# Performance work log

Measured on AMD Instinct MI355X. Metric: run time of the kernel, lower is better.

The kernel has to match this reference:

```python
import jax, jax.numpy as jnp
import numpy as np

H = 8      # num_attention_heads
DH = 96    # attention_head_size
LN_EPS = 1e-5


def setup_inputs() -> dict:
    key = jax.random.key(0)
    ks = jax.random.split(key, 12)
    B, S, D = 2, 768, 768
    sc = 0.02
    return {
        "hidden_states": jax.random.normal(ks[0], (B, S, D), jnp.float32),
        "distance_matrix": jax.random.uniform(ks[1], (B, S, S), jnp.float32) * 20.0,
        "angle_matrix": jax.random.uniform(ks[2], (B, S, S), jnp.float32) * np.pi,
        "attention_mask": jnp.ones((B, S), jnp.float32),
        "Wq": jax.random.normal(ks[3], (D, D), jnp.float32) * sc,
        "bq": jnp.zeros((D,), jnp.float32),
        "Wk": jax.random.normal(ks[4], (D, D), jnp.float32) * sc,
        "bk": jnp.zeros((D,), jnp.float32),
        "Wv": jax.random.normal(ks[5], (D, D), jnp.float32) * sc,
        "bv": jnp.zeros((D,), jnp.float32),
        "Wd": jax.random.normal(ks[6], (DH,), jnp.float32) * sc,
        "bd": jnp.zeros((DH,), jnp.float32),
        "Wa": jax.random.normal(ks[7], (DH,), jnp.float32) * sc,
        "ba": jnp.zeros((DH,), jnp.float32),
        "Wo": jax.random.normal(ks[8], (D, D), jnp.float32) * sc,
        "bo": jnp.zeros((D,), jnp.float32),
        "ln_g": jnp.ones((D,), jnp.float32),
        "ln_b": jnp.zeros((D,), jnp.float32),
    }


def _heads(x, B, S):
    # [B,S,D] -> [B,H,S,DH]
    return x.reshape(B, S, H, DH).transpose(0, 2, 1, 3)


def reference(hidden_states, distance_matrix, angle_matrix, attention_mask,
              Wq, bq, Wk, bk, Wv, bv, Wd, bd, Wa, ba, Wo, bo, ln_g, ln_b):
    B, S, D = hidden_states.shape
    q = _heads(hidden_states @ Wq.T + bq, B, S)   # [B,H,S,DH]
    k = _heads(hidden_states @ Wk.T + bk, B, S)
    v = _heads(hidden_states @ Wv.T + bv, B, S)

    scores = jnp.einsum('bhid,bhjd->bhij', q, k) / jnp.sqrt(jnp.float32(DH))

    # distance / angle relative-position biases: emb[b,i,j,:] = dist[b,i,j]*Wd + bd
    dist_emb = distance_matrix[..., None] * Wd + bd   # [B,S,S,DH]
    scores = scores + jnp.einsum('bhid,bijd->bhij', q, dist_emb)
    ang_emb = angle_matrix[..., None] * Wa + ba       # [B,S,S,DH]
    scores = scores + jnp.einsum('bhid,bijd->bhij', q, ang_emb)

    # key mask, broadcast over heads and query positions
    scores = scores + (1.0 - attention_mask)[:, None, None, :] * -10000.0

    probs = jax.nn.softmax(scores, axis=-1)           # [B,H,S,S]
    ctx = jnp.einsum('bhij,bhjd->bhid', probs, v)
    ctx = ctx.transpose(0, 2, 1, 3).reshape(B, S, D)  # [B,S,D]

    out = ctx @ Wo.T + bo
    x = out + hidden_states
    mu = jnp.mean(x, axis=-1, keepdims=True)
    var = jnp.var(x, axis=-1, keepdims=True)
    out = (x - mu) * jax.lax.rsqrt(var + LN_EPS) * ln_g + ln_b
    return out, probs
```

## Files before the change

### kernel.cpp

```cpp
#include <hip/hip_runtime.h>
#include <stdint.h>

#define B_  2
#define S_  768
#define D_  768
#define H_  8
#define DH_ 96

typedef unsigned short ushort_t;
typedef __bf16 bf16x8 __attribute__((ext_vector_type(8)));
typedef float  f32x4  __attribute__((ext_vector_type(4)));

__device__ inline ushort_t f2bf(float f) {
    union { float f; unsigned int u; } v; v.f = f;
    unsigned int u = v.u;
    unsigned int r = u + 0x7fffu + ((u >> 16) & 1u);
    return (ushort_t)(r >> 16);
}
__device__ inline float bf2f(ushort_t u) {
    union { unsigned int i; float f; } c; c.i = ((unsigned int)u) << 16;
    return c.f;
}

__device__ inline void glds16(const void* gp, void* lp) {
    auto g = reinterpret_cast<const __attribute__((address_space(1))) uint32_t*>(
        reinterpret_cast<uintptr_t>(gp));
    auto l = reinterpret_cast<__attribute__((address_space(3))) uint32_t*>(
        reinterpret_cast<uintptr_t>(lp));
    __builtin_amdgcn_global_load_lds(g, l, 16, 0, 0);
}

__global__ __launch_bounds__(256) void k_convert(
        const float* __restrict__ X, const float* __restrict__ Wq,
        const float* __restrict__ Wk, const float* __restrict__ Wv,
        const float* __restrict__ Wo,
        ushort_t* __restrict__ Xb, ushort_t* __restrict__ Wb) {
    const int NX4 = (B_ * S_ * D_) / 4;
    const int NW4 = (D_ * D_) / 4;
    int i = blockIdx.x * blockDim.x + threadIdx.x;
    float4 v;
    ushort_t* dst;
    if (i < NX4) {
        v = ((const float4*)X)[i];
        dst = Xb + i * 4;
    } else {
        int wi = i - NX4;
        int sel = wi / NW4;
        int off = wi - sel * NW4;
        const float* src = (sel == 0) ? Wq : (sel == 1) ? Wk : (sel == 2) ? Wv : Wo;
        v = ((const float4*)src)[off];
        dst = Wb + wi * 4;
    }
    ushort4 o;
    o.x = f2bf(v.x); o.y = f2bf(v.y); o.z = f2bf(v.z); o.w = f2bf(v.w);
    *(ushort4*)dst = o;
}

__device__ inline void gemm64_dbuf(
        const ushort_t* __restrict__ A, int lda,
        const ushort_t* __restrict__ Bt, int ldb,
        int K, int m0, int n0,
        ushort_t* As, ushort_t* Bs, f32x4 acc[2][2]) {
    const int tid  = threadIdx.x;
    const int lane = tid & 63, wave = tid >> 6;
    const int wm = (wave >> 1) * 32, wn = (wave & 1) * 32;
    const int fr = lane & 15, fk = (lane >> 4) * 8;
    const ushort_t* Ap = A  + (size_t)(m0 + wave * 16 + (lane >> 2)) * lda + (lane & 3) * 8;
    const ushort_t* Bp = Bt + (size_t)(n0 + wave * 16 + (lane >> 2)) * ldb + (lane & 3) * 8;
    glds16(Ap, As + wave * 512);
    glds16(Bp, Bs + wave * 512);
    for (int kt = 0; kt < K; kt += 32) {
        const int cur = (kt >> 5) & 1;
        __syncthreads();
        if (kt + 32 < K) {
            glds16(Ap + kt + 32, As + (cur ^ 1) * 2048 + wave * 512);
            glds16(Bp + kt + 32, Bs + (cur ^ 1) * 2048 + wave * 512);
        }
        const ushort_t* Ab = As + cur * 2048;
        const ushort_t* Bb = Bs + cur * 2048;
        bf16x8 a0 = *(const bf16x8*)&Ab[(wm      + fr) * 32 + fk];
        bf16x8 a1 = *(const bf16x8*)&Ab[(wm + 16 + fr) * 32 + fk];
        bf16x8 b0 = *(const bf16x8*)&Bb[(wn      + fr) * 32 + fk];
        bf16x8 b1 = *(const bf16x8*)&Bb[(wn + 16 + fr) * 32 + fk];
        acc[0][0] = __builtin_amdgcn_mfma_f32_16x16x32_bf16(a0, b0, acc[0][0], 0, 0, 0);
        acc[0][1] = __builtin_amdgcn_mfma_f32_16x16x32_bf16(a0, b1, acc[0][1], 0, 0, 0);
        acc[1][0] = __builtin_amdgcn_mfma_f32_16x16x32_bf16(a1, b0, acc[1][0], 0, 0, 0);
        acc[1][1] = __builtin_amdgcn_mfma_f32_16x16x32_bf16(a1, b1, acc[1][1], 0, 0, 0);
    }
}

__global__ __launch_bounds__(256) void k_qkv(
        const ushort_t* __restrict__ Xb, const ushort_t* __restrict__ Wb,
        const float* __restrict__ bq, const float* __restrict__ bk,
        const float* __restrict__ bv,
        ushort_t* __restrict__ Qb, ushort_t* __restrict__ Kb,
        ushort_t* __restrict__ Vtb) {
    __shared__ __align__(16) ushort_t As[2 * 64 * 32];
    __shared__ __align__(16) ushort_t Bs[2 * 64 * 32];
    f32x4 acc[2][2];
    #pragma unroll
    for (int i = 0; i < 2; i++)
        #pragma unroll
        for (int j = 0; j < 2; j++) acc[i][j] = (f32x4){0.f, 0.f, 0.f, 0.f};
    const int m0 = blockIdx.y * 64, n0 = blockIdx.x * 64;
    gemm64_dbuf(Xb, D_, Wb, D_, D_, m0, n0, As, Bs, acc);
    const int lane = threadIdx.x & 63, wave = threadIdx.x >> 6;
    const int wm = (wave >> 1) * 32, wn = (wave & 1) * 32;
    #pragma unroll
    for (int ni = 0; ni < 2; ni++) {
        int gcol = n0 + wn + ni * 16 + (lane & 15);
        int gsel = gcol / D_, d768 = gcol - gsel * D_;
        int h = d768 / DH_, d = d768 - h * DH_;
        float bias = (gsel == 0 ? bq : (gsel == 1 ? bk : bv))[d768];
        #pragma unroll
        for (int mi = 0; mi < 2; mi++) {
            int grow0 = m0 + wm + mi * 16 + (lane >> 4) * 4;
            int b = grow0 / S_, s0 = grow0 - b * S_;
            int bh = b * H_ + h;
            if (gsel == 2) {
                ushort4 o4;
                o4.x = f2bf(acc[mi][ni][0] + bias);
                o4.y = f2bf(acc[mi][ni][1] + bias);
                o4.z = f2bf(acc[mi][ni][2] + bias);
                o4.w = f2bf(acc[mi][ni][3] + bias);
                *(ushort4*)&Vtb[((size_t)bh * DH_ + d) * S_ + s0] = o4;
            } else if (gsel == 1) {
                #pragma unroll
                for (int r = 0; r < 4; r++) {
                    ushort_t ob = f2bf(acc[mi][ni][r] + bias);
                    Kb[(((size_t)bh * 12 + (d >> 3)) * S_ + s0 + r) * 8 + (d & 7)] = ob;
                }
            } else {
                #pragma unroll
                for (int r = 0; r < 4; r++) {
                    ushort_t ob = f2bf(acc[mi][ni][r] + bias);
                    Qb[((size_t)bh * S_ + s0 + r) * DH_ + d] = ob;
                }
            }
        }
    }
}

__global__ __launch_bounds__(256) void k_qcoef(
        const ushort_t* __restrict__ Qb,
        const float* __restrict__ Wd, const float* __restrict__ bd,
        const float* __restrict__ Wa, const float* __restrict__ ba,
        float* __restrict__ qcoef) {
    const int wave = threadIdx.x >> 6, lane = threadIdx.x & 63;
    const int row = blockIdx.x * 4 + wave;
    const ushort_t* q = Qb + (size_t)row * DH_;
    float e0 = bf2f(q[lane]);
    float c0 = e0 * Wd[lane];
    float c1 = e0 * Wa[lane];
    float c2 = e0 * (bd[lane] + ba[lane]);
    if (lane < 32) {
        int d = 64 + lane;
        float e1 = bf2f(q[d]);
        c0 += e1 * Wd[d];
        c1 += e1 * Wa[d];
        c2 += e1 * (bd[d] + ba[d]);
    }
    #pragma unroll
    for (int o = 32; o > 0; o >>= 1) {
        c0 += __shfl_down(c0, o);
        c1 += __shfl_down(c1, o);
        c2 += __shfl_down(c2, o);
    }
    if (lane == 0) {
        qcoef[row * 3 + 0] = c0;
        qcoef[row * 3 + 1] = c1;
        qcoef[row * 3 + 2] = c2;
    }
}

#define FL1B 20480
#define VBUF 24576
__global__ __launch_bounds__(256, 3) void k_flash(
        const ushort_t* __restrict__ Qb, const ushort_t* __restrict__ Kb,
        const ushort_t* __restrict__ Vtb, const float* __restrict__ qcoef,
        const float* __restrict__ distm, const float* __restrict__ angm,
        const float* __restrict__ mask,
        float* __restrict__ probs, ushort_t* __restrict__ Ctxb) {
    __shared__ __align__(16) char sm[2 * VBUF + 512];
    float* mstat = (float*)(sm + 2 * VBUF);
    float* lstat = (float*)(sm + 2 * VBUF + 256);
    const int idx = blockIdx.x;
    const int h = idx / 96, rem = idx - h * 96;
    const int b = rem / 48, r0 = (rem - b * 48) * 16;
    const int bh = b * H_ + h;
    const int tid = threadIdx.x, lane = tid & 63, w = tid >> 6;
    const int frn = lane & 15, g = lane >> 4;
    const ushort_t* Qbh = Qb + (size_t)bh * S_ * DH_;
    const ushort_t* Kbh = Kb + (size_t)bh * 12 * S_ * 8;
    const ushort_t* Vbh = Vtb + (size_t)bh * DH_ * S_;

    auto stage = [&](int c) {
        char* bufc = sm + (c & 1) * FL1B;
        ushort_t* Ks = (ushort_t*)bufc;
        #pragma unroll
        for (int t = 0; t < 3; ++t) {
            int grp = w * 3 + t;
            glds16(Kbh + (((size_t)grp * S_ + c * 64 + lane) << 3), Ks + grp * 512);
        }
        int row = 4 * w + g;
        int colb = (frn ^ (row & 7)) << 2;
        size_t src = ((size_t)b * S_ + r0 + row) * S_ + c * 64 + colb;
        glds16(distm + src, (float*)(bufc + 12288) + w * 256);
        glds16(angm  + src, (float*)(bufc + 16384) + w * 256);
    };
    auto stage_v = [&](int p) {
        ushort_t* Vs = (ushort_t*)(sm + (p & 1) * VBUF);
        const int c0 = p * 128;
        #pragma unroll
        for (int t = 0; t < 6; ++t) {
            int q = w * 6 + t;
            int d = 4 * q + (lane >> 4);
            int ug = (lane & 15) ^ (d & 15);
            glds16(Vbh + (size_t)d * S_ + c0 + ug * 8, Vs + q * 512);
        }
    };

    stage(0);

    bf16x8 aq0, aq1, aq2;
    {
        const ushort_t* qp = Qbh + (size_t)(r0 + frn) * DH_ + g * 8;
        aq0 = *(const bf16x8*)qp;
        aq1 = *(const bf16x8*)(qp + 32);
        aq2 = *(const bf16x8*)(qp + 64);
    }
    float qc0, qc1, qc2;
    {
        const float* qp = qcoef + ((size_t)bh * S_ + r0 + frn) * 3;
        qc0 = qp[0]; qc1 = qp[1]; qc2 = qp[2];
    }
    const float isq = 0.10206207261596577f;
    const int dswz = ((4 * w + g) ^ (frn & 7)) << 2;
    const int jrow = (16 * w + frn) * 8;

    f32x4 acc[12];
    __syncthreads();
    #pragma unroll
    for (int c = 0; c < 12; ++c) {
        if (c < 11) stage(c + 1);
        char* bufc = sm + (c & 1) * FL1B;
        const ushort_t* Ks = (const ushort_t*)bufc;
        const float* Dd = (const float*)(bufc + 12288);
        const float* Da = (const float*)(bufc + 16384);
        bf16x8 k0 = *(const bf16x8*)&Ks[(g    ) * 512 + jrow];
        bf16x8 k1 = *(const bf16x8*)&Ks[(g + 4) * 512 + jrow];
        bf16x8 k2 = *(const bf16x8*)&Ks[(g + 8) * 512 + jrow];
        f32x4 ca = (f32x4){0.f, 0.f, 0.f, 0.f};
        ca = __builtin_amdgcn_mfma_f32_16x16x32_bf16(k0, aq0, ca, 0, 0, 0);
        ca = __builtin_amdgcn_mfma_f32_16x16x32_bf16(k1, aq1, ca, 0, 0, 0);
        ca = __builtin_amdgcn_mfma_f32_16x16x32_bf16(k2, aq2, ca, 0, 0, 0);
        float4 d4 = *(const float4*)(Dd + frn * 64 + dswz);
        float4 a4 = *(const float4*)(Da + frn * 64 + dswz);
        float4 m4 = *(const float4*)(mask + b * S_ + c * 64 + w * 16 + g * 4);
        f32x4 o;
        o[0] = ca[0] * isq + d4.x * qc0 + a4.x * qc1 + qc2 + (1.f - m4.x) * -10000.f;
        o[1] = ca[1] * isq + d4.y * qc0 + a4.y * qc1 + qc2 + (1.f - m4.y) * -10000.f;
        o[2] = ca[2] * isq + d4.z * qc0 + a4.z * qc1 + qc2 + (1.f - m4.z) * -10000.f;
        o[3] = ca[3] * isq + d4.w * qc0 + a4.w * qc1 + qc2 + (1.f - m4.w) * -10000.f;
        acc[c] = o;
        __syncthreads();
    }

    stage_v(0);
    float mx = -1e30f;
    #pragma unroll
    for (int c = 0; c < 12; ++c)
        #pragma unroll
        for (int r = 0; r < 4; ++r) mx = fmaxf(mx, acc[c][r]);
    mx = fmaxf(mx, __shfl_xor(mx, 16));
    mx = fmaxf(mx, __shfl_xor(mx, 32));
    if (g == 0) mstat[w * 16 + frn] = mx;
    __syncthreads();
    float mf = fmaxf(fmaxf(mstat[frn], mstat[16 + frn]),
                     fmaxf(mstat[32 + frn], mstat[48 + frn]));
    float sum = 0.f;
    #pragma unroll
    for (int c = 0; c < 12; ++c)
        #pragma unroll
        for (int r = 0; r < 4; ++r) {
            float e = __expf(acc[c][r] - mf);
            acc[c][r] = e;
            sum += e;
        }
    sum += __shfl_xor(sum, 16);
    sum += __shfl_xor(sum, 32);
    if (g == 0) lstat[w * 16 + frn] = sum;
    __syncthreads();
    float inv = 1.f / (lstat[frn] + lstat[16 + frn] + lstat[32 + frn] + lstat[48 + frn]);

    f32x4 accO[6];
    #pragma unroll
    for (int i = 0; i < 6; ++i) accO[i] = (f32x4){0.f, 0.f, 0.f, 0.f};
    float* prow = probs + ((size_t)bh * S_ + r0 + frn) * S_ + w * 16 + g * 4;
    const int vsub = (g & 1) << 2;
    const int u0 = 2 * w + (g >> 1);
    #pragma unroll
    for (int p = 0; p < 6; ++p) {
        if (p < 5) stage_v(p + 1);
        const ushort_t* Vs = (const ushort_t*)(sm + (p & 1) * VBUF);
        const int c = 2 * p;
        float4 pw;
        pw.x = acc[c][0] * inv; pw.y = acc[c][1] * inv;
        pw.z = acc[c][2] * inv; pw.w = acc[c][3] * inv;
        *(float4*)(prow + c * 64) = pw;
        pw.x = acc[c + 1][0] * inv; pw.y = acc[c + 1][1] * inv;
        pw.z = acc[c + 1][2] * inv; pw.w = acc[c + 1][3] * inv;
        *(float4*)(prow + (c + 1) * 64) = pw;
        union { bf16x8 v; ushort_t u[8]; } pa;
        #pragma unroll
        for (int r = 0; r < 4; ++r) {
            pa.u[r]     = f2bf(acc[c][r]);
            pa.u[r + 4] = f2bf(acc[c + 1][r]);
        }
        #pragma unroll
        for (int nt = 0; nt < 6; ++nt) {
            int d = nt * 16 + frn;
            const ushort_t* vr = Vs + d * 128 + vsub;
            union { bf16x8 v; uint2 q2[2]; } vb;
            vb.q2[0] = *(const uint2*)(vr + (((u0    ) ^ frn) << 3));
            vb.q2[1] = *(const uint2*)(vr + (((u0 + 8) ^ frn) << 3));
            accO[nt] = __builtin_amdgcn_mfma_f32_16x16x32_bf16(pa.v, vb.v, accO[nt], 0, 0, 0);
        }
        __syncthreads();
    }

    float* ctxred = (float*)sm;
    {
        int zr = tid >> 4, zc = tid & 15;
        #pragma unroll
        for (int i = 0; i < 6; ++i) ctxred[zr * 100 + i * 16 + zc] = 0.f;
    }
    __syncthreads();
    #pragma unroll
    for (int nt = 0; nt < 6; ++nt)
        #pragma unroll
        for (int r = 0; r < 4; ++r)
            atomicAdd(&ctxred[(4 * g + r) * 100 + nt * 16 + frn], accO[nt][r]);
    __syncthreads();
    {
        int zr = tid >> 4, zc = tid & 15;
        float ivr = 1.f / (lstat[zr] + lstat[16 + zr] + lstat[32 + zr] + lstat[48 + zr]);
        ushort_t* crow = Ctxb + ((size_t)b * S_ + r0 + zr) * D_ + h * DH_;
        #pragma unroll
        for (int i = 0; i < 6; ++i)
            crow[i * 16 + zc] = f2bf(ctxred[zr * 100 + i * 16 + zc] * ivr);
    }
}

__global__ __launch_bounds__(256) void k_out(
        const ushort_t* __restrict__ Ctxb, const ushort_t* __restrict__ Wob,
        const float* __restrict__ bo, const float* __restrict__ hidden,
        float* __restrict__ xbuf) {
    __shared__ __align__(16) ushort_t As[2 * 64 * 32];
    __shared__ __align__(16) ushort_t Bs[2 * 64 * 32];
    f32x4 acc[2][2];
    #pragma unroll
    for (int i = 0; i < 2; i++)
        #pragma unroll
        for (int j = 0; j < 2; j++) acc[i][j] = (f32x4){0.f, 0.f, 0.f, 0.f};
    const int m0 = blockIdx.y * 64, n0 = blockIdx.x * 64;
    gemm64_dbuf(Ctxb, D_, Wob, D_, D_, m0, n0, As, Bs, acc);
    const int lane = threadIdx.x & 63, wave = threadIdx.x >> 6;
    const int wm = (wave >> 1) * 32, wn = (wave & 1) * 32;
    #pragma unroll
    for (int ni = 0; ni < 2; ni++) {
        int gcol = n0 + wn + ni * 16 + (lane & 15);
        float bias = bo[gcol];
        #pragma unroll
        for (int mi = 0; mi < 2; mi++) {
            #pragma unroll
            for (int r = 0; r < 4; r++) {
                int grow = m0 + wm + mi * 16 + (lane >> 4) * 4 + r;
                xbuf[(size_t)grow * D_ + gcol] =
                    acc[mi][ni][r] + bias + hidden[(size_t)grow * D_ + gcol];
            }
        }
    }
}

__global__ __launch_bounds__(256) void k_ln(
        const float* __restrict__ xbuf, const float* __restrict__ g,
        const float* __restrict__ bb, float* __restrict__ out) {
    const float* x = xbuf + (size_t)blockIdx.x * D_;
    const int t = threadIdx.x;
    float a0 = x[t], a1 = x[t + 256], a2 = x[t + 512];
    float s = a0 + a1 + a2;
    float ss = a0 * a0 + a1 * a1 + a2 * a2;
    __shared__ float r1[4], r2[4];
    #pragma unroll
    for (int o = 32; o > 0; o >>= 1) { s += __shfl_down(s, o); ss += __shfl_down(ss, o); }
    if ((t & 63) == 0) { r1[t >> 6] = s; r2[t >> 6] = ss; }
    __syncthreads();
    float ts = r1[0] + r1[1] + r1[2] + r1[3];
    float tss = r2[0] + r2[1] + r2[2] + r2[3];
    float mu = ts * (1.0f / D_);
    float var = tss * (1.0f / D_) - mu * mu;
    float rstd = rsqrtf(var + 1e-5f);
    float* o = out + (size_t)blockIdx.x * D_;
    o[t]       = (a0 - mu) * rstd * g[t]       + bb[t];
    o[t + 256] = (a1 - mu) * rstd * g[t + 256] + bb[t + 256];
    o[t + 512] = (a2 - mu) * rstd * g[t + 512] + bb[t + 512];
}

extern "C" void kernel_launch(void* const* d_in, const int* in_sizes, int n_in,
                              void* d_out, int out_size, void* d_ws, size_t ws_size,
                              hipStream_t stream) {
    const float* X     = (const float*)d_in[0];
    const float* distm = (const float*)d_in[1];
    const float* angm  = (const float*)d_in[2];
    const float* mask  = (const float*)d_in[3];
    const float* Wq    = (const float*)d_in[4];
    const float* bq    = (const float*)d_in[5];
    const float* Wk    = (const float*)d_in[6];
    const float* bk    = (const float*)d_in[7];
    const float* Wv    = (const float*)d_in[8];
    const float* bv    = (const float*)d_in[9];
    const float* Wd    = (const float*)d_in[10];
    const float* bd    = (const float*)d_in[11];
    const float* Wa    = (const float*)d_in[12];
    const float* ba    = (const float*)d_in[13];
    const float* Wo    = (const float*)d_in[14];
    const float* bo    = (const float*)d_in[15];
    const float* ln_g  = (const float*)d_in[16];
    const float* ln_b  = (const float*)d_in[17];

    float* outp  = (float*)d_out;
    float* probs = (float*)d_out + (size_t)B_ * S_ * D_;

    char* ws = (char*)d_ws;
    ushort_t* Xb    = (ushort_t*)(ws + 0);
    ushort_t* Wb    = (ushort_t*)(ws + 2359296);
    ushort_t* Qb    = (ushort_t*)(ws + 7077888);
    ushort_t* Kb    = (ushort_t*)(ws + 9437184);
    ushort_t* Vtb   = (ushort_t*)(ws + 11796480);
    ushort_t* Ctxb  = (ushort_t*)(ws + 14155776);
    float*    qcoef = (float*)   (ws + 16515072);
    float*    xbuf  = (float*)   (ws + 16662528);

    k_convert<<<3456, 256, 0, stream>>>(X, Wq, Wk, Wv, Wo, Xb, Wb);
    k_qkv<<<dim3(36, 24), 256, 0, stream>>>(Xb, Wb, bq, bk, bv, Qb, Kb, Vtb);
    k_qcoef<<<3072, 256, 0, stream>>>(Qb, Wd, bd, Wa, ba, qcoef);
    k_flash<<<768, 256, 0, stream>>>(Qb, Kb, Vtb, qcoef, distm, angm, mask, probs, Ctxb);
    k_out<<<dim3(12, 24), 256, 0, stream>>>(Ctxb, Wb + (size_t)2304 * 768, bo, X, xbuf);
    k_ln<<<1536, 256, 0, stream>>>(xbuf, ln_g, ln_b, outp);
}
```

Baseline: 190.6 us.

## Pre-convert distance/angle matrices to fp16, enlarge QKV GEMM tiles, remap flash blocks

The distance and angle matrices are converted to fp16 in the conversion kernel, so the attention kernel stages half as many bytes per tile through LDS, using a new swizzle. The QKV projection moves from 64x64 to 128x128 tiles with a 4x4 MFMA fragment grid per wave for more data reuse. The flash kernel's block index now interleaves batch and head in its low bits. The extra conversion pass reads the fp32 matrices and writes fp16 copies, which adds global traffic that may cancel the savings, and fp16 rounding slightly perturbs the bias terms.

```diff
diff --git a/kernel.cpp b/kernel.cpp
--- a/kernel.cpp
+++ b/kernel.cpp
@@ -10,6 +10,7 @@
 typedef unsigned short ushort_t;
 typedef __bf16 bf16x8 __attribute__((ext_vector_type(8)));
 typedef float  f32x4  __attribute__((ext_vector_type(4)));
+typedef _Float16 f16x4 __attribute__((ext_vector_type(4)));
 
 __device__ inline ushort_t f2bf(float f) {
     union { float f; unsigned int u; } v; v.f = f;
@@ -20,6 +21,9 @@
 __device__ inline float bf2f(ushort_t u) {
     union { unsigned int i; float f; } c; c.i = ((unsigned int)u) << 16;
     return c.f;
+}
+__device__ inline ushort_t f2h(float f) {
+    union { _Float16 h; ushort_t u; } c; c.h = (_Float16)f; return c.u;
 }
 
 __device__ inline void glds16(const void* gp, void* lp) {
@@ -33,26 +37,40 @@
 __global__ __launch_bounds__(256) void k_convert(
         const float* __restrict__ X, const float* __restrict__ Wq,
         const float* __restrict__ Wk, const float* __restrict__ Wv,
-        const float* __restrict__ Wo,
-        ushort_t* __restrict__ Xb, ushort_t* __restrict__ Wb) {
+        const float* __restrict__ Wo, const float* __restrict__ distm,
+        const float* __restrict__ angm,
+        ushort_t* __restrict__ Xb, ushort_t* __restrict__ Wb,
+        ushort_t* __restrict__ Dh, ushort_t* __restrict__ Ah) {
     const int NX4 = (B_ * S_ * D_) / 4;
     const int NW4 = (D_ * D_) / 4;
+    const int NWall = 4 * NW4;
+    const int ND4 = (B_ * S_ * S_) / 4;
     int i = blockIdx.x * blockDim.x + threadIdx.x;
     float4 v;
     ushort_t* dst;
+    bool h16 = false;
     if (i < NX4) {
         v = ((const float4*)X)[i];
         dst = Xb + i * 4;
-    } else {
+    } else if (i < NX4 + NWall) {
         int wi = i - NX4;
         int sel = wi / NW4;
         int off = wi - sel * NW4;
         const float* src = (sel == 0) ? Wq : (sel == 1) ? Wk : (sel == 2) ? Wv : Wo;
         v = ((const float4*)src)[off];
         dst = Wb + wi * 4;
+    } else if (i < NX4 + NWall + ND4) {
+        int off = i - NX4 - NWall;
+        v = ((const float4*)distm)[off];
+        dst = Dh + off * 4; h16 = true;
+    } else {
+        int off = i - NX4 - NWall - ND4;
+        v = ((const float4*)angm)[off];
+        dst = Ah + off * 4; h16 = true;
     }
     ushort4 o;
-    o.x = f2bf(v.x); o.y = f2bf(v.y); o.z = f2bf(v.z); o.w = f2bf(v.w);
+    if (h16) { o.x = f2h(v.x); o.y = f2h(v.y); o.z = f2h(v.z); o.w = f2h(v.w); }
+    else     { o.x = f2bf(v.x); o.y = f2bf(v.y); o.z = f2bf(v.z); o.w = f2bf(v.w); }
     *(ushort4*)dst = o;
 }
 
@@ -95,47 +113,71 @@
         const float* __restrict__ bv,
         ushort_t* __restrict__ Qb, ushort_t* __restrict__ Kb,
         ushort_t* __restrict__ Vtb) {
-    __shared__ __align__(16) ushort_t As[2 * 64 * 32];
-    __shared__ __align__(16) ushort_t Bs[2 * 64 * 32];
-    f32x4 acc[2][2];
-    #pragma unroll
-    for (int i = 0; i < 2; i++)
-        #pragma unroll
-        for (int j = 0; j < 2; j++) acc[i][j] = (f32x4){0.f, 0.f, 0.f, 0.f};
-    const int m0 = blockIdx.y * 64, n0 = blockIdx.x * 64;
-    gemm64_dbuf(Xb, D_, Wb, D_, D_, m0, n0, As, Bs, acc);
-    const int lane = threadIdx.x & 63, wave = threadIdx.x >> 6;
-    const int wm = (wave >> 1) * 32, wn = (wave & 1) * 32;
-    #pragma unroll
-    for (int ni = 0; ni < 2; ni++) {
-        int gcol = n0 + wn + ni * 16 + (lane & 15);
+    __shared__ __align__(16) ushort_t As[2][128 * 32];
+    __shared__ __align__(16) ushort_t Bs[2][128 * 32];
+    const int tid = threadIdx.x, lane = tid & 63, w = tid >> 6;
+    const int m0 = blockIdx.y * 128, n0 = blockIdx.x * 128;
+    const int frn = lane & 15, fko = (lane >> 4) * 8, frg4 = (lane >> 4) * 4;
+    const int wm = (w >> 1) * 64, wn = (w & 1) * 64;
+    const int srow = lane >> 2, scol = (lane & 3) * 8;
+    f32x4 acc[4][4];
+    #pragma unroll
+    for (int i = 0; i < 4; i++)
+        #pragma unroll
+        for (int j = 0; j < 4; j++) acc[i][j] = (f32x4){0.f, 0.f, 0.f, 0.f};
+    auto stageAB = [&](int kt, int buf) {
+        #pragma unroll
+        for (int t = 0; t < 2; ++t) {
+            int ins = w * 2 + t;
+            int row = ins * 16 + srow;
+            glds16(Xb + (size_t)(m0 + row) * D_ + kt + scol, &As[buf][ins * 512]);
+            glds16(Wb + (size_t)(n0 + row) * D_ + kt + scol, &Bs[buf][ins * 512]);
+        }
+    };
+    stageAB(0, 0);
+    for (int kt = 0; kt < D_; kt += 32) {
+        const int cur = (kt >> 5) & 1;
+        __syncthreads();
+        if (kt + 32 < D_) stageAB(kt + 32, cur ^ 1);
+        bf16x8 af[4], bfr[4];
+        #pragma unroll
+        for (int i = 0; i < 4; ++i) {
+            af[i]  = *(const bf16x8*)&As[cur][(wm + i * 16 + frn) * 32 + fko];
+            bfr[i] = *(const bf16x8*)&Bs[cur][(wn + i * 16 + frn) * 32 + fko];
+        }
+        #pragma unroll
+        for (int i = 0; i < 4; ++i)
+            #pragma unroll
+            for (int j = 0; j < 4; ++j)
+                acc[i][j] = __builtin_amdgcn_mfma_f32_16x16x32_bf16(af[i], bfr[j], acc[i][j], 0, 0, 0);
+    }
+    #pragma unroll
+    for (int j = 0; j < 4; ++j) {
+        int gcol = n0 + wn + j * 16 + frn;
         int gsel = gcol / D_, d768 = gcol - gsel * D_;
         int h = d768 / DH_, d = d768 - h * DH_;
         float bias = (gsel == 0 ? bq : (gsel == 1 ? bk : bv))[d768];
         #pragma unroll
-        for (int mi = 0; mi < 2; mi++) {
-            int grow0 = m0 + wm + mi * 16 + (lane >> 4) * 4;
+        for (int i = 0; i < 4; ++i) {
+            int grow0 = m0 + wm + i * 16 + frg4;
             int b = grow0 / S_, s0 = grow0 - b * S_;
             int bh = b * H_ + h;
             if (gsel == 2) {
                 ushort4 o4;
-                o4.x = f2bf(acc[mi][ni][0] + bias);
-                o4.y = f2bf(acc[mi][ni][1] + bias);
-                o4.z = f2bf(acc[mi][ni][2] + bias);
-                o4.w = f2bf(acc[mi][ni][3] + bias);
+                o4.x = f2bf(acc[i][j][0] + bias);
+                o4.y = f2bf(acc[i][j][1] + bias);
+                o4.z = f2bf(acc[i][j][2] + bias);
+                o4.w = f2bf(acc[i][j][3] + bias);
                 *(ushort4*)&Vtb[((size_t)bh * DH_ + d) * S_ + s0] = o4;
             } else if (gsel == 1) {
                 #pragma unroll
-                for (int r = 0; r < 4; r++) {
-                    ushort_t ob = f2bf(acc[mi][ni][r] + bias);
-                    Kb[(((size_t)bh * 12 + (d >> 3)) * S_ + s0 + r) * 8 + (d & 7)] = ob;
-                }
+                for (int r = 0; r < 4; r++)
+                    Kb[(((size_t)bh * 12 + (d >> 3)) * S_ + s0 + r) * 8 + (d & 7)] =
+                        f2bf(acc[i][j][r] + bias);
             } else {
                 #pragma unroll
-                for (int r = 0; r < 4; r++) {
-                    ushort_t ob = f2bf(acc[mi][ni][r] + bias);
-                    Qb[((size_t)bh * S_ + s0 + r) * DH_ + d] = ob;
-                }
+                for (int r = 0; r < 4; r++)
+                    Qb[((size_t)bh * S_ + s0 + r) * DH_ + d] = f2bf(acc[i][j][r] + bias);
             }
         }
     }
@@ -173,21 +215,21 @@
     }
 }
 
-#define FL1B 20480
+#define FL1B 16384
 #define VBUF 24576
 __global__ __launch_bounds__(256, 3) void k_flash(
         const ushort_t* __restrict__ Qb, const ushort_t* __restrict__ Kb,
         const ushort_t* __restrict__ Vtb, const float* __restrict__ qcoef,
-        const float* __restrict__ distm, const float* __restrict__ angm,
+        const ushort_t* __restrict__ Dh, const ushort_t* __restrict__ Ah,
         const float* __restrict__ mask,
         float* __restrict__ probs, ushort_t* __restrict__ Ctxb) {
     __shared__ __align__(16) char sm[2 * VBUF + 512];
     float* mstat = (float*)(sm + 2 * VBUF);
     float* lstat = (float*)(sm + 2 * VBUF + 256);
     const int idx = blockIdx.x;
-    const int h = idx / 96, rem = idx - h * 96;
-    const int b = rem / 48, r0 = (rem - b * 48) * 16;
-    const int bh = b * H_ + h;
+    const int bh = idx & 15, t = idx >> 4;
+    const int b = bh >> 3, h = bh & 7;
+    const int r0 = t * 16;
     const int tid = threadIdx.x, lane = tid & 63, w = tid >> 6;
     const int frn = lane & 15, g = lane >> 4;
     const ushort_t* Qbh = Qb + (size_t)bh * S_ * DH_;
@@ -198,22 +240,22 @@
         char* bufc = sm + (c & 1) * FL1B;
         ushort_t* Ks = (ushort_t*)bufc;
         #pragma unroll
-        for (int t = 0; t < 3; ++t) {
-            int grp = w * 3 + t;
+        for (int tt = 0; tt < 3; ++tt) {
+            int grp = w * 3 + tt;
             glds16(Kbh + (((size_t)grp * S_ + c * 64 + lane) << 3), Ks + grp * 512);
         }
-        int row = 4 * w + g;
-        int colb = (frn ^ (row & 7)) << 2;
-        size_t src = ((size_t)b * S_ + r0 + row) * S_ + c * 64 + colb;
-        glds16(distm + src, (float*)(bufc + 12288) + w * 256);
-        glds16(angm  + src, (float*)(bufc + 16384) + w * 256);
+        int row8 = ((w & 1) << 3) + (lane >> 3);
+        int usrc = (2 * (lane & 7)) ^ (row8 & 14);
+        const ushort_t* srcm = (w >> 1) ? Ah : Dh;
+        glds16(srcm + ((size_t)(b * S_ + r0 + row8)) * S_ + c * 64 + usrc * 4,
+               bufc + 12288 + ((w >> 1) << 11) + ((w & 1) << 10));
     };
     auto stage_v = [&](int p) {
         ushort_t* Vs = (ushort_t*)(sm + (p & 1) * VBUF);
         const int c0 = p * 128;
         #pragma unroll
-        for (int t = 0; t < 6; ++t) {
-            int q = w * 6 + t;
+        for (int tt = 0; tt < 6; ++tt) {
+            int q = w * 6 + tt;
             int d = 4 * q + (lane >> 4);
             int ug = (lane & 15) ^ (d & 15);
             glds16(Vbh + (size_t)d * S_ + c0 + ug * 8, Vs + q * 512);
@@ -235,7 +277,7 @@
         qc0 = qp[0]; qc1 = qp[1]; qc2 = qp[2];
     }
     const float isq = 0.10206207261596577f;
-    const int dswz = ((4 * w + g) ^ (frn & 7)) << 2;
+    const int daswz = (((w * 4 + g) ^ (frn & 14)) << 2);
     const int jrow = (16 * w + frn) * 8;
 
     f32x4 acc[12];
@@ -245,8 +287,6 @@
         if (c < 11) stage(c + 1);
         char* bufc = sm + (c & 1) * FL1B;
         const ushort_t* Ks = (const ushort_t*)bufc;
-        const float* Dd = (const float*)(bufc + 12288);
-        const float* Da = (const float*)(bufc + 16384);
         bf16x8 k0 = *(const bf16x8*)&Ks[(g    ) * 512 + jrow];
         bf16x8 k1 = *(const bf16x8*)&Ks[(g + 4) * 512 + jrow];
         bf16x8 k2 = *(const bf16x8*)&Ks[(g + 8) * 512 + jrow];
@@ -254,14 +294,14 @@
         ca = __builtin_amdgcn_mfma_f32_16x16x32_bf16(k0, aq0, ca, 0, 0, 0);
         ca = __builtin_amdgcn_mfma_f32_16x16x32_bf16(k1, aq1, ca, 0, 0, 0);
         ca = __builtin_amdgcn_mfma_f32_16x16x32_bf16(k2, aq2, ca, 0, 0, 0);
-        float4 d4 = *(const float4*)(Dd + frn * 64 + dswz);
-        float4 a4 = *(const float4*)(Da + frn * 64 + dswz);
+        f16x4 d4 = *(const f16x4*)((const ushort_t*)(bufc + 12288) + frn * 64 + daswz);
+        f16x4 a4 = *(const f16x4*)((const ushort_t*)(bufc + 14336) + frn * 64 + daswz);
         float4 m4 = *(const float4*)(mask + b * S_ + c * 64 + w * 16 + g * 4);
         f32x4 o;
-        o[0] = ca[0] * isq + d4.x * qc0 + a4.x * qc1 + qc2 + (1.f - m4.x) * -10000.f;
-        o[1] = ca[1] * isq + d4.y * qc0 + a4.y * qc1 + qc2 + (1.f - m4.y) * -10000.f;
-        o[2] = ca[2] * isq + d4.z * qc0 + a4.z * qc1 + qc2 + (1.f - m4.z) * -10000.f;
-        o[3] = ca[3] * isq + d4.w * qc0 + a4.w * qc1 + qc2 + (1.f - m4.w) * -10000.f;
+        o[0] = ca[0] * isq + (float)d4[0] * qc0 + (float)a4[0] * qc1 + qc2 + (1.f - m4.x) * -10000.f;
+        o[1] = ca[1] * isq + (float)d4[1] * qc0 + (float)a4[1] * qc1 + qc2 + (1.f - m4.y) * -10000.f;
+        o[2] = ca[2] * isq + (float)d4[2] * qc0 + (float)a4[2] * qc1 + qc2 + (1.f - m4.z) * -10000.f;
+        o[3] = ca[3] * isq + (float)d4[3] * qc0 + (float)a4[3] * qc1 + qc2 + (1.f - m4.w) * -10000.f;
         acc[c] = o;
         __syncthreads();
     }
@@ -441,11 +481,13 @@
     ushort_t* Ctxb  = (ushort_t*)(ws + 14155776);
     float*    qcoef = (float*)   (ws + 16515072);
     float*    xbuf  = (float*)   (ws + 16662528);
-
-    k_convert<<<3456, 256, 0, stream>>>(X, Wq, Wk, Wv, Wo, Xb, Wb);
-    k_qkv<<<dim3(36, 24), 256, 0, stream>>>(Xb, Wb, bq, bk, bv, Qb, Kb, Vtb);
+    ushort_t* Dh    = (ushort_t*)(ws + 16662528);
+    ushort_t* Ah    = (ushort_t*)(ws + 16662528 + 2359296);
+
+    k_convert<<<5760, 256, 0, stream>>>(X, Wq, Wk, Wv, Wo, distm, angm, Xb, Wb, Dh, Ah);
+    k_qkv<<<dim3(18, 12), 256, 0, stream>>>(Xb, Wb, bq, bk, bv, Qb, Kb, Vtb);
     k_qcoef<<<3072, 256, 0, stream>>>(Qb, Wd, bd, Wa, ba, qcoef);
-    k_flash<<<768, 256, 0, stream>>>(Qb, Kb, Vtb, qcoef, distm, angm, mask, probs, Ctxb);
+    k_flash<<<768, 256, 0, stream>>>(Qb, Kb, Vtb, qcoef, Dh, Ah, mask, probs, Ctxb);
     k_out<<<dim3(12, 24), 256, 0, stream>>>(Ctxb, Wb + (size_t)2304 * 768, bo, X, xbuf);
     k_ln<<<1536, 256, 0, stream>>>(xbuf, ln_g, ln_b, outp);
 }
```

After: 191.7 us. No clear change (+0.6%).
